# Kernel optimization log

Hardware: AMD Instinct MI355X
Metric: run time of the kernel (lower is better)

The kernel has to match this reference:

```python
import jax, jax.numpy as jnp
import numpy as np

WS = (2, 7, 7)        # window_size (D, H, W)
DIM = 192
NHEADS = 6
NW = 64               # number of windows per image
BATCH = 32            # images -> B_ = NW*BATCH
CPB_HIDDEN = 512


def _make_buffers():
    # continuous relative coords table, shape (1, 2Wd-1, 2Wh-1, 2Ww-1, 3)
    axes = [np.arange(-(w - 1), w, dtype=np.float32) for w in WS]
    table = np.stack(np.meshgrid(*axes, indexing='ij'), axis=-1)[None]
    for i in range(3):
        table[..., i] /= (WS[i] - 1)
    table *= 8
    table = np.sign(table) * np.log2(np.abs(table) + 1.0) / np.log2(8)
    # relative position index, shape (N, N)
    coords = np.stack(np.meshgrid(np.arange(WS[0]), np.arange(WS[1]), np.arange(WS[2]), indexing='ij'))
    cf = coords.reshape(3, -1)
    rel = (cf[:, :, None] - cf[:, None, :]).transpose(1, 2, 0).astype(np.int64)
    rel[..., 0] += WS[0] - 1
    rel[..., 1] += WS[1] - 1
    rel[..., 2] += WS[2] - 1
    rel[..., 0] *= (2 * WS[1] - 1) * (2 * WS[2] - 1)
    rel[..., 1] *= 2 * WS[2] - 1
    rpi = rel.sum(-1)
    return jnp.asarray(table, jnp.float32), jnp.asarray(rpi, jnp.int32)


def setup_inputs() -> dict:
    key = jax.random.key(0)
    ks = jax.random.split(key, 10)
    N = WS[0] * WS[1] * WS[2]
    B_ = NW * BATCH
    x = jax.random.normal(ks[0], (B_, N, DIM), jnp.float32)
    mask = jax.random.normal(ks[1], (NW, N, N), jnp.float32)
    qkv_w = jax.random.normal(ks[2], (3 * DIM, DIM), jnp.float32) * 0.02
    qkv_b = jnp.zeros((3 * DIM,), jnp.float32)
    logit_scale = jnp.log(10.0 * jnp.ones((NHEADS, 1, 1), jnp.float32))
    cpb_w1 = jax.random.normal(ks[3], (CPB_HIDDEN, 3), jnp.float32) * 0.02
    cpb_b1 = jnp.zeros((CPB_HIDDEN,), jnp.float32)
    cpb_w2 = jax.random.normal(ks[4], (NHEADS, CPB_HIDDEN), jnp.float32) * 0.02
    proj_w = jax.random.normal(ks[5], (DIM, DIM), jnp.float32) * 0.02
    proj_b = jnp.zeros((DIM,), jnp.float32)
    rel_coords_table, rel_pos_index = _make_buffers()
    return dict(x=x, mask=mask, qkv_w=qkv_w, qkv_b=qkv_b, logit_scale=logit_scale,
                cpb_w1=cpb_w1, cpb_b1=cpb_b1, cpb_w2=cpb_w2,
                proj_w=proj_w, proj_b=proj_b,
                rel_coords_table=rel_coords_table, rel_pos_index=rel_pos_index)


def _l2norm(t, eps=1e-12):
    # F.normalize(dim=-1): x / max(||x||, eps)
    n = jnp.sqrt(jnp.sum(t * t, axis=-1, keepdims=True))
    return t / jnp.maximum(n, eps)


def reference(x, mask, qkv_w, qkv_b, logit_scale, cpb_w1, cpb_b1, cpb_w2,
              proj_w, proj_b, rel_coords_table, rel_pos_index):
    B_, N, C = x.shape
    H = logit_scale.shape[0]
    hd = C // H
    qkv = (x @ qkv_w.T + qkv_b).reshape(B_, N, 3, H, hd).transpose(2, 0, 3, 1, 4)
    q, k, v = qkv[0], qkv[1], qkv[2]          # (B_, H, N, hd)
    attn = jnp.einsum('bhnd,bhmd->bhnm', _l2norm(q), _l2norm(k))
    scale = jnp.exp(jnp.minimum(logit_scale, jnp.log(jnp.float32(100.0))))  # (H,1,1)
    attn = attn * scale
    # continuous position bias: MLP over coords table, gather, 16*sigmoid
    hidden = jax.nn.relu(rel_coords_table @ cpb_w1.T + cpb_b1)
    tbl = (hidden @ cpb_w2.T).reshape(-1, H)
    bias = tbl[rel_pos_index.reshape(-1)].reshape(N, N, H).transpose(2, 0, 1)
    attn = attn + (16.0 * jax.nn.sigmoid(bias))[None]
    nW = mask.shape[0]
    attn = attn.reshape(B_ // nW, nW, H, N, N) + mask[None, :, None]
    attn = jax.nn.softmax(attn.reshape(B_, H, N, N), axis=-1)
    out = jnp.einsum('bhnm,bhmd->bhnd', attn, v).transpose(0, 2, 1, 3).reshape(B_, N, C)
    return out @ proj_w.T + proj_b
```

## Files before the change

kernel.cpp:

```cpp
#include <hip/hip_runtime.h>
#include <hip/hip_bf16.h>
#include <hip/hip_fp16.h>

typedef __attribute__((ext_vector_type(8))) short short8;
typedef __attribute__((ext_vector_type(4))) float f32x4;
typedef __attribute__((ext_vector_type(4))) unsigned short us4;

#define MFMA16(a, b, c) __builtin_amdgcn_mfma_f32_16x16x32_bf16(a, b, c, 0, 0, 0)
#define LN100 4.605170185988091f

__device__ __forceinline__ short f2bf(float f) {
    unsigned u = __float_as_uint(f);
    unsigned r = (u + 0x7fffu + ((u >> 16) & 1u)) >> 16;
    return (short)r;
}
__device__ __forceinline__ float h2f(unsigned short u) {
    __half_raw r; r.x = u;
    return __half2float(__half(r));
}


__global__ __launch_bounds__(256) void k_wcvt(const float* qkv_w, const float* proj_w,
                                              short* wq, short* wp) {
    int i = blockIdx.x * 256 + threadIdx.x;
    if (i < 576 * 192) wq[i] = f2bf(qkv_w[i]);
    else {
        int j = i - 576 * 192;
        if (j < 192 * 192) wp[j] = f2bf(proj_w[j]);
    }
}

__global__ __launch_bounds__(64) void k_tbl(const float* tab, const float* w1, const float* b1,
                                            const float* w2, float* tbl) {
    int e = blockIdx.x;
    int t = threadIdx.x;
    float c0 = tab[e * 3 + 0], c1 = tab[e * 3 + 1], c2 = tab[e * 3 + 2];
    float acc[6] = {0.f, 0.f, 0.f, 0.f, 0.f, 0.f};
    for (int u = t; u < 512; u += 64) {
        float hv = c0 * w1[u * 3 + 0] + c1 * w1[u * 3 + 1] + c2 * w1[u * 3 + 2] + b1[u];
        hv = fmaxf(hv, 0.f);
        #pragma unroll
        for (int hh = 0; hh < 6; ++hh) acc[hh] += hv * w2[hh * 512 + u];
    }
    #pragma unroll
    for (int hh = 0; hh < 6; ++hh) {
        float v = acc[hh];
        for (int off = 32; off > 0; off >>= 1) v += __shfl_xor(v, off, 64);
        if (t == 0) tbl[e * 6 + hh] = v;
    }
}

__global__ __launch_bounds__(256) void k_bm(const float* tbl, const int* rpi, const float* mask,
                                            __half* bm) {
    int i = blockIdx.x * 256 + threadIdx.x;
    if (i >= 64 * 6 * 98 * 112) return;
    int k = i % 112;
    int q = (i / 112) % 98;
    int h = (i / (112 * 98)) % 6;
    int w = i / (112 * 98 * 6);
    float v;
    if (k < 98) {
        float t = tbl[rpi[q * 98 + k] * 6 + h];
        v = 16.f / (1.f + expf(-t)) + mask[(w * 98 + q) * 98 + k];
    } else v = -60000.f;
    bm[i] = __float2half(v);
}

__global__ __launch_bounds__(896) void k_fused(const float* x, const short* wq, const float* qkv_b,
                                               const float* lsc, const short* wp, const float* proj_b,
                                               const __half* bm, float* outp) {
    __shared__ short lds[79872];
    short* Qs = lds;
    short* Ks = lds + 21504;
    short* VT = lds + 43008;
    short* Bs = lds + 67584;

    const int tid = threadIdx.x;
    const int wv = tid >> 6;
    const int lane = tid & 63;
    const int l16 = lane & 15, q4 = lane >> 4;
    const int rg = wv >> 1;
    const int hf = wv & 1;
    const int b = blockIdx.x;
    const int w = b & 63;
    const f32x4 zz = {0.f, 0.f, 0.f, 0.f};

    {
        short8 z = {0, 0, 0, 0, 0, 0, 0, 0};
        #pragma unroll
        for (int it = 0; it < 4; ++it) {
            int c = tid + it * 896;
            if (c < 3072) *(short8*)&VT[c * 8] = z;
        }
    }
    short8 af[6];
    {
        int arow = rg * 16 + l16; if (arow > 97) arow = 97;
        const float* xp = x + ((size_t)b * 98 + arow) * 192 + q4 * 8;
        #pragma unroll
        for (int ks = 0; ks < 6; ++ks) {
            float4 f0 = *(const float4*)(xp + ks * 32);
            float4 f1 = *(const float4*)(xp + ks * 32 + 4);
            union { int i4[4]; short8 s; } u;
            asm("v_cvt_pk_bf16_f32 %0, %1, %2" : "=v"(u.i4[0]) : "v"(f0.x), "v"(f0.y));
            asm("v_cvt_pk_bf16_f32 %0, %1, %2" : "=v"(u.i4[1]) : "v"(f0.z), "v"(f0.w));
            asm("v_cvt_pk_bf16_f32 %0, %1, %2" : "=v"(u.i4[2]) : "v"(f1.x), "v"(f1.y));
            asm("v_cvt_pk_bf16_f32 %0, %1, %2" : "=v"(u.i4[3]) : "v"(f1.z), "v"(f1.w));
            af[ks] = u.s;
        }
    }
    short8 t0, t1;
    {
        int c1 = tid + 896;
        t0 = *(const short8*)(wq + (tid / 24) * 192 + (tid % 24) * 8);
        if (c1 < 1536) t1 = *(const short8*)(wq + (c1 / 24) * 192 + (c1 % 24) * 8);
    }
    __syncthreads();
    {
        int c1 = tid + 896;
        *(short8*)&Bs[(tid / 24) * 192 + (((tid % 24) ^ ((tid / 24) & 7)) << 3)] = t0;
        if (c1 < 1536) *(short8*)&Bs[(c1 / 24) * 192 + (((c1 % 24) ^ ((c1 / 24) & 7)) << 3)] = t1;
    }
    __syncthreads();

    const int row_w = rg * 16 + q4 * 4;
    #pragma unroll 1
    for (int nt = 0; nt < 9; ++nt) {
        if (nt < 8) {
            const short* wn = wq + (nt + 1) * 64 * 192;
            int c1 = tid + 896;
            t0 = *(const short8*)(wn + (tid / 24) * 192 + (tid % 24) * 8);
            if (c1 < 1536) t1 = *(const short8*)(wn + (c1 / 24) * 192 + (c1 % 24) * 8);
        }
        f32x4 acc[2] = {zz, zz};
        #pragma unroll
        for (int ks = 0; ks < 6; ++ks)
            #pragma unroll
            for (int cf = 0; cf < 2; ++cf) {
                short8 bf = *(const short8*)&Bs[((hf * 2 + cf) * 16 + l16) * 192 +
                                                (((ks * 4 + q4) ^ (l16 & 7)) << 3)];
                acc[cf] = MFMA16(af[ks], bf, acc[cf]);
            }
        {
            int slot = nt * 2 + hf;
            int which = slot / 6;
            int h = slot - which * 6;
            float bia0 = qkv_b[slot * 32 + l16];
            float bia1 = qkv_b[slot * 32 + 16 + l16];
            float sc = 1.0f;
            if (which == 0) sc = __expf(fminf(lsc[h], LN100));
            #pragma unroll
            for (int i = 0; i < 4; ++i) {
                float v0 = acc[0][i] + bia0;
                float v1 = acc[1][i] + bia1;
                if (which < 2) {
                    float ss = v0 * v0 + v1 * v1;
                    ss += __shfl_xor(ss, 1, 16);
                    ss += __shfl_xor(ss, 2, 16);
                    ss += __shfl_xor(ss, 4, 16);
                    ss += __shfl_xor(ss, 8, 16);
                    float rn = sc / fmaxf(sqrtf(ss), 1e-12f);
                    v0 *= rn; v1 *= rn;
                }
                int row = row_w + i;
                if (which == 2) {
                    int swz = (((row >> 3) ^ (l16 & 7)) << 3) + (row & 7);
                    VT[h * 4096 + l16 * 128 + swz]        = f2bf(v0);
                    VT[h * 4096 + (l16 + 16) * 128 + swz] = f2bf(v1);
                } else {
                    short* T = (which == 0) ? Qs : Ks;
                    int c0i = h * 32 + l16, c1i = c0i + 16;
                    T[row * 192 + (((c0i >> 3) ^ (row & 7)) << 3) + (c0i & 7)] = f2bf(v0);
                    T[row * 192 + (((c1i >> 3) ^ (row & 7)) << 3) + (c1i & 7)] = f2bf(v1);
                }
            }
        }
        __syncthreads();
        if (nt < 8) {
            int c1 = tid + 896;
            *(short8*)&Bs[(tid / 24) * 192 + (((tid % 24) ^ ((tid / 24) & 7)) << 3)] = t0;
            if (c1 < 1536) *(short8*)&Bs[(c1 / 24) * 192 + (((c1 % 24) ^ ((c1 / 24) & 7)) << 3)] = t1;
            __syncthreads();
        }
    }

    const int rq = rg * 16 + l16;
    const int qc = rq < 98 ? rq : 97;
    const int srcA = ((q4 & 1) * 2) * 16 + l16;
    const int srcB = srcA + 16;
    const bool hi = (q4 & 2) != 0;

    #pragma unroll 1
    for (int j = 0; j < 3; ++j) {
        const int h = hf * 3 + j;
        const __half* bmp = bm + (((size_t)w * 6 + h) * 98 + qc) * 112;
        us4 bh[7];
        #pragma unroll
        for (int ct = 0; ct < 7; ++ct) bh[ct] = *(const us4*)(bmp + ct * 16 + q4 * 4);
        short8 qf = *(const short8*)&Qs[rq * 192 + (((h * 4 + q4) ^ (l16 & 7)) << 3)];
        f32x4 cc[7];
        #pragma unroll
        for (int ct = 0; ct < 7; ++ct) {
            int rk = ct * 16 + l16;
            short8 kf = *(const short8*)&Ks[rk * 192 + (((h * 4 + q4) ^ (l16 & 7)) << 3)];
            cc[ct] = MFMA16(kf, qf, zz);
        }
        float mx = -1e30f;
        #pragma unroll
        for (int ct = 0; ct < 7; ++ct)
            #pragma unroll
            for (int i = 0; i < 4; ++i) {
                float s = cc[ct][i] + h2f(bh[ct][i]);
                cc[ct][i] = s;
                mx = fmaxf(mx, s);
            }
        mx = fmaxf(mx, __shfl_xor(mx, 16, 64));
        mx = fmaxf(mx, __shfl_xor(mx, 32, 64));
        float sm = 0.f;
        #pragma unroll
        for (int ct = 0; ct < 7; ++ct)
            #pragma unroll
            for (int i = 0; i < 4; ++i) {
                float e = __expf(cc[ct][i] - mx);
                cc[ct][i] = e;
                sm += e;
            }
        sm += __shfl_xor(sm, 16, 64);
        sm += __shfl_xor(sm, 32, 64);
        float ri = 1.f / sm;
        int W[8][2];
        W[7][0] = 0; W[7][1] = 0;
        #pragma unroll
        for (int ct = 0; ct < 7; ++ct) {
            float a0 = cc[ct][0] * ri, a1 = cc[ct][1] * ri;
            float a2 = cc[ct][2] * ri, a3 = cc[ct][3] * ri;
            asm("v_cvt_pk_bf16_f32 %0, %1, %2" : "=v"(W[ct][0]) : "v"(a0), "v"(a1));
            asm("v_cvt_pk_bf16_f32 %0, %1, %2" : "=v"(W[ct][1]) : "v"(a2), "v"(a3));
        }
        f32x4 o0 = zz, o1 = zz;
        #pragma unroll
        for (int km = 0; km < 4; ++km) {
            int A0 = __shfl(W[2 * km][0], srcA, 64), B0 = __shfl(W[2 * km + 1][0], srcA, 64);
            int A1 = __shfl(W[2 * km][1], srcA, 64), B1 = __shfl(W[2 * km + 1][1], srcA, 64);
            int A2 = __shfl(W[2 * km][0], srcB, 64), B2 = __shfl(W[2 * km + 1][0], srcB, 64);
            int A3 = __shfl(W[2 * km][1], srcB, 64), B3 = __shfl(W[2 * km + 1][1], srcB, 64);
            union { int i4[4]; short8 s; } ua;
            ua.i4[0] = hi ? B0 : A0;
            ua.i4[1] = hi ? B1 : A1;
            ua.i4[2] = hi ? B2 : A2;
            ua.i4[3] = hi ? B3 : A3;
            int sA = h * 4096 + l16 * 128 + (((km * 4 + q4) ^ (l16 & 7)) << 3);
            short8 bv0 = *(const short8*)&VT[sA];
            short8 bv1 = *(const short8*)&VT[sA + 2048];
            o0 = MFMA16(ua.s, bv0, o0);
            o1 = MFMA16(ua.s, bv1, o1);
        }
        __syncthreads();
        #pragma unroll
        for (int i = 0; i < 4; ++i) {
            int q = row_w + i;
            VT[h * 4096 + q * 32 + l16]      = f2bf(o0[i]);
            VT[h * 4096 + q * 32 + 16 + l16] = f2bf(o1[i]);
        }
    }

    {
        short8 pwst[6];
        #pragma unroll
        for (int it = 0; it < 6; ++it) {
            int c = tid + it * 896;
            if (c < 4608) pwst[it] = *(const short8*)(wp + (c / 24) * 192 + (c % 24) * 8);
        }
        #pragma unroll
        for (int it = 0; it < 6; ++it) {
            int c = tid + it * 896;
            if (c < 4608)
                *(short8*)&lds[(c / 24) * 192 + (((c % 24) ^ ((c / 24) & 7)) << 3)] = pwst[it];
        }
    }
    __syncthreads();
    {
        short8 pa[6];
        #pragma unroll
        for (int ks = 0; ks < 6; ++ks)
            pa[ks] = *(const short8*)&VT[ks * 4096 + rq * 32 + q4 * 8];
        f32x4 pacc[6] = {zz, zz, zz, zz, zz, zz};
        #pragma unroll
        for (int ks = 0; ks < 6; ++ks)
            #pragma unroll
            for (int cf = 0; cf < 6; ++cf) {
                short8 bf = *(const short8*)&lds[((hf * 6 + cf) * 16 + l16) * 192 +
                                                 (((ks * 4 + q4) ^ (l16 & 7)) << 3)];
                pacc[cf] = MFMA16(pa[ks], bf, pacc[cf]);
            }
        #pragma unroll
        for (int cf = 0; cf < 6; ++cf) {
            int cg = (hf * 6 + cf) * 16 + l16;
            float bia = proj_b[cg];
            #pragma unroll
            for (int i = 0; i < 4; ++i) {
                int q = row_w + i;
                if (q < 98)
                    outp[((size_t)b * 98 + q) * 192 + cg] = pacc[cf][i] + bia;
            }
        }
    }
}

extern "C" void kernel_launch(void* const* d_in, const int* in_sizes, int n_in,
                              void* d_out, int out_size, void* d_ws, size_t ws_size,
                              hipStream_t stream) {
    const float* x    = (const float*)d_in[0];
    const float* mask = (const float*)d_in[1];
    const float* qkvw = (const float*)d_in[2];
    const float* qkvb = (const float*)d_in[3];
    const float* lsc  = (const float*)d_in[4];
    const float* w1   = (const float*)d_in[5];
    const float* b1   = (const float*)d_in[6];
    const float* w2   = (const float*)d_in[7];
    const float* pw   = (const float*)d_in[8];
    const float* pb   = (const float*)d_in[9];
    const float* tab  = (const float*)d_in[10];
    const int*   rpi  = (const int*)d_in[11];

    char* ws = (char*)d_ws;
    short*  wq  = (short*)(ws + 0);
    short*  wp  = (short*)(ws + 221184);
    float*  tbl = (float*)(ws + 294912);
    __half* bm  = (__half*)(ws + 307200);
    float*  outp = (float*)d_out;

    k_wcvt<<<576, 256, 0, stream>>>(qkvw, pw, wq, wp);
    k_tbl<<<507, 64, 0, stream>>>(tab, w1, b1, w2, tbl);
    k_bm<<<16464, 256, 0, stream>>>(tbl, rpi, mask, bm);
    k_fused<<<2048, 896, 0, stream>>>(x, wq, qkvb, lsc, wp, pb, bm, outp);
}
```

Baseline: 377.2 us.

## Pre-swizzle bf16 weights in global memory and store bias-mask as fp32

The weight conversion kernel now writes the qkv and proj weights directly in the XOR-swizzled LDS layout. The fused kernel can then copy weight tiles linearly, without per-thread div/mod and swizzle arithmetic. Separately, the bias+mask buffer is stored as fp32 instead of fp16, which removes the half-to-float conversions in the softmax path. The trade-off is doubled bias-mask traffic: each fused block reads 16-byte vectors instead of 8-byte ones, and the prep kernel writes twice the bytes.

```diff
diff --git a/kernel.cpp b/kernel.cpp
--- a/kernel.cpp
+++ b/kernel.cpp
@@ -4,7 +4,6 @@
 
 typedef __attribute__((ext_vector_type(8))) short short8;
 typedef __attribute__((ext_vector_type(4))) float f32x4;
-typedef __attribute__((ext_vector_type(4))) unsigned short us4;
 
 #define MFMA16(a, b, c) __builtin_amdgcn_mfma_f32_16x16x32_bf16(a, b, c, 0, 0, 0)
 #define LN100 4.605170185988091f
@@ -14,19 +13,23 @@
     unsigned r = (u + 0x7fffu + ((u >> 16) & 1u)) >> 16;
     return (short)r;
 }
-__device__ __forceinline__ float h2f(unsigned short u) {
-    __half_raw r; r.x = u;
-    return __half2float(__half(r));
-}
 
 
 __global__ __launch_bounds__(256) void k_wcvt(const float* qkv_w, const float* proj_w,
-                                              short* wq, short* wp) {
+                                              short* wq_sw, short* wp_sw) {
     int i = blockIdx.x * 256 + threadIdx.x;
-    if (i < 576 * 192) wq[i] = f2bf(qkv_w[i]);
-    else {
+    if (i < 576 * 192) {
+        int c = i / 192, k = i % 192;
+        int nt = c >> 6, r = c & 63;
+        int L = nt * 12288 + r * 192 + ((((k >> 3) ^ (r & 7)) << 3) | (k & 7));
+        wq_sw[L] = f2bf(qkv_w[i]);
+    } else {
         int j = i - 576 * 192;
-        if (j < 192 * 192) wp[j] = f2bf(proj_w[j]);
+        if (j < 192 * 192) {
+            int r = j / 192, k = j % 192;
+            int L = r * 192 + ((((k >> 3) ^ (r & 7)) << 3) | (k & 7));
+            wp_sw[L] = f2bf(proj_w[j]);
+        }
     }
 }
 
@@ -51,7 +54,7 @@
 }
 
 __global__ __launch_bounds__(256) void k_bm(const float* tbl, const int* rpi, const float* mask,
-                                            __half* bm) {
+                                            float* bm) {
     int i = blockIdx.x * 256 + threadIdx.x;
     if (i >= 64 * 6 * 98 * 112) return;
     int k = i % 112;
@@ -63,12 +66,12 @@
         float t = tbl[rpi[q * 98 + k] * 6 + h];
         v = 16.f / (1.f + expf(-t)) + mask[(w * 98 + q) * 98 + k];
     } else v = -60000.f;
-    bm[i] = __float2half(v);
+    bm[i] = v;
 }
 
 __global__ __launch_bounds__(896) void k_fused(const float* x, const short* wq, const float* qkv_b,
                                                const float* lsc, const short* wp, const float* proj_b,
-                                               const __half* bm, float* outp) {
+                                               const float* bm, float* outp) {
     __shared__ short lds[79872];
     short* Qs = lds;
     short* Ks = lds + 21504;
@@ -111,15 +114,13 @@
     }
     short8 t0, t1;
     {
-        int c1 = tid + 896;
-        t0 = *(const short8*)(wq + (tid / 24) * 192 + (tid % 24) * 8);
-        if (c1 < 1536) t1 = *(const short8*)(wq + (c1 / 24) * 192 + (c1 % 24) * 8);
+        t0 = *(const short8*)(wq + tid * 8);
+        if (tid < 640) t1 = *(const short8*)(wq + (tid + 896) * 8);
     }
     __syncthreads();
     {
-        int c1 = tid + 896;
-        *(short8*)&Bs[(tid / 24) * 192 + (((tid % 24) ^ ((tid / 24) & 7)) << 3)] = t0;
-        if (c1 < 1536) *(short8*)&Bs[(c1 / 24) * 192 + (((c1 % 24) ^ ((c1 / 24) & 7)) << 3)] = t1;
+        *(short8*)&Bs[tid * 8] = t0;
+        if (tid < 640) *(short8*)&Bs[(tid + 896) * 8] = t1;
     }
     __syncthreads();
 
@@ -127,10 +128,9 @@
     #pragma unroll 1
     for (int nt = 0; nt < 9; ++nt) {
         if (nt < 8) {
-            const short* wn = wq + (nt + 1) * 64 * 192;
-            int c1 = tid + 896;
-            t0 = *(const short8*)(wn + (tid / 24) * 192 + (tid % 24) * 8);
-            if (c1 < 1536) t1 = *(const short8*)(wn + (c1 / 24) * 192 + (c1 % 24) * 8);
+            const short* wn = wq + (nt + 1) * 12288;
+            t0 = *(const short8*)(wn + tid * 8);
+            if (tid < 640) t1 = *(const short8*)(wn + (tid + 896) * 8);
         }
         f32x4 acc[2] = {zz, zz};
         #pragma unroll
@@ -177,9 +177,8 @@
         }
         __syncthreads();
         if (nt < 8) {
-            int c1 = tid + 896;
-            *(short8*)&Bs[(tid / 24) * 192 + (((tid % 24) ^ ((tid / 24) & 7)) << 3)] = t0;
-            if (c1 < 1536) *(short8*)&Bs[(c1 / 24) * 192 + (((c1 % 24) ^ ((c1 / 24) & 7)) << 3)] = t1;
+            *(short8*)&Bs[tid * 8] = t0;
+            if (tid < 640) *(short8*)&Bs[(tid + 896) * 8] = t1;
             __syncthreads();
         }
     }
@@ -193,10 +192,10 @@
     #pragma unroll 1
     for (int j = 0; j < 3; ++j) {
         const int h = hf * 3 + j;
-        const __half* bmp = bm + (((size_t)w * 6 + h) * 98 + qc) * 112;
-        us4 bh[7];
-        #pragma unroll
-        for (int ct = 0; ct < 7; ++ct) bh[ct] = *(const us4*)(bmp + ct * 16 + q4 * 4);
+        const float* bmp = bm + (((size_t)w * 6 + h) * 98 + qc) * 112;
+        f32x4 bh[7];
+        #pragma unroll
+        for (int ct = 0; ct < 7; ++ct) bh[ct] = *(const f32x4*)(bmp + ct * 16 + q4 * 4);
         short8 qf = *(const short8*)&Qs[rq * 192 + (((h * 4 + q4) ^ (l16 & 7)) << 3)];
         f32x4 cc[7];
         #pragma unroll
@@ -210,7 +209,7 @@
         for (int ct = 0; ct < 7; ++ct)
             #pragma unroll
             for (int i = 0; i < 4; ++i) {
-                float s = cc[ct][i] + h2f(bh[ct][i]);
+                float s = cc[ct][i] + bh[ct][i];
                 cc[ct][i] = s;
                 mx = fmaxf(mx, s);
             }
@@ -269,13 +268,12 @@
         #pragma unroll
         for (int it = 0; it < 6; ++it) {
             int c = tid + it * 896;
-            if (c < 4608) pwst[it] = *(const short8*)(wp + (c / 24) * 192 + (c % 24) * 8);
+            if (c < 4608) pwst[it] = *(const short8*)(wp + c * 8);
         }
         #pragma unroll
         for (int it = 0; it < 6; ++it) {
             int c = tid + it * 896;
-            if (c < 4608)
-                *(short8*)&lds[(c / 24) * 192 + (((c % 24) ^ ((c / 24) & 7)) << 3)] = pwst[it];
+            if (c < 4608) *(short8*)&lds[c * 8] = pwst[it];
         }
     }
     __syncthreads();
@@ -327,7 +325,7 @@
     short*  wq  = (short*)(ws + 0);
     short*  wp  = (short*)(ws + 221184);
     float*  tbl = (float*)(ws + 294912);
-    __half* bm  = (__half*)(ws + 307200);
+    float*  bm  = (float*)(ws + 307200);
     float*  outp = (float*)d_out;
 
     k_wcvt<<<576, 256, 0, stream>>>(qkvw, pw, wq, wp);
```

Measured after the change: 353.6 us (median of 3 runs). 6.2% less time.
